# Kernel tuning notes

Measured on AMD Instinct MI355X. Metric: run time of the kernel, lower is better.

The kernel has to match this reference:

```python
import jax, jax.numpy as jnp
import numpy as np

TH = 0.01  # threshold from init
H = 56
W = 56


def setup_inputs() -> dict:
    key = jax.random.key(0)
    k1, k2 = jax.random.split(key)
    x = jax.random.uniform(k1, (32, 512, 56, 56), dtype=jnp.float32)
    conv_w = jax.random.normal(k2, (512, 1, 1, 1), dtype=jnp.float32)
    scale = jnp.ones((1,), dtype=jnp.float32)
    wf = jnp.ones((1,), dtype=jnp.float32)
    return {"x": x, "conv_w": conv_w, "scale": scale, "wf": wf}


def reference(x, conv_w, scale, wf):
    B, C, _, _ = x.shape
    # per-channel spatial mean: alpha[b,c] = sum_hw x / (H*W)
    alpha = jnp.sum(x, axis=(2, 3)) / (H * W)  # [B, C]
    # channel-weighted spatial sum, averaged over channels -> saliency [B, H, W]
    sal = jnp.einsum('bchw,bc->bhw', x, alpha) / C
    # conv1x1 with 1 input channel: broadcastmul by per-output-channel scalar
    w = conv_w.reshape(1, -1, 1, 1)                 # [1, Cout, 1, 1]
    fm = sal[:, None, :, :] * w                     # [B, Cout, H, W]
    fm = jax.nn.relu(fm)
    fm = jnp.where(fm > TH, fm, 0.0)                # nn.Threshold(th, 0)
    return 1.0 - wf * jax.nn.sigmoid(scale * fm)
```

## Files before the change

kernel.cpp:

```cpp
#include <hip/hip_runtime.h>
#include <hip/hip_bf16.h>

#define B 32
#define C 512
#define HW 3136
#define HW4 784
#define TH 0.01f
#define CPB 16
#define CPW 4
#define NPG 32

typedef float fx4 __attribute__((ext_vector_type(4)));

__global__ __launch_bounds__(256, 4) void partial_kernel(const float* __restrict__ x,
                                                         float* __restrict__ out) {
    const int b  = blockIdx.y;
    const int cg = blockIdx.x;
    const int t  = threadIdx.x;
    const int l  = t & 63;
    const int w  = t >> 6;

    const fx4* __restrict__ xb = (const fx4*)(x + (size_t)b * C * HW);

    fx4 acc[13];
    #pragma unroll
    for (int j = 0; j < 13; ++j) acc[j] = (fx4)0.f;

    const int cbase = cg * CPB + w * CPW;
    for (int i = 0; i < CPW; ++i) {
        const fx4* __restrict__ p = xb + (size_t)(cbase + i) * HW4;
        fx4 v[13];
        #pragma unroll
        for (int j = 0; j < 12; ++j) v[j] = __builtin_nontemporal_load(p + l + 64 * j);
        if (l < 16) v[12] = __builtin_nontemporal_load(p + l + 768);

        float s = 0.f;
        #pragma unroll
        for (int j = 0; j < 12; ++j) s += (v[j].x + v[j].y) + (v[j].z + v[j].w);
        if (l < 16) s += (v[12].x + v[12].y) + (v[12].z + v[12].w);
        #pragma unroll
        for (int off = 1; off < 64; off <<= 1) s += __shfl_xor(s, off);
        const float a = s * (1.0f / (float)HW);

        #pragma unroll
        for (int j = 0; j < 12; ++j) acc[j] += v[j] * a;
        if (l < 16) acc[12] += v[12] * a;
    }

    __shared__ fx4 lds[3][HW4];
    if (w > 0) {
        #pragma unroll
        for (int j = 0; j < 12; ++j) lds[w - 1][l + 64 * j] = acc[j];
        if (l < 16) lds[w - 1][l + 768] = acc[12];
    }
    __syncthreads();
    if (w == 0) {
        fx4* __restrict__ dst = (fx4*)(out + (size_t)b * C * HW) + (size_t)cg * HW4;
        #pragma unroll
        for (int j = 0; j < 12; ++j) {
            const int col = l + 64 * j;
            dst[col] = ((acc[j] + lds[0][col]) + (lds[1][col] + lds[2][col]));
        }
        if (l < 16) {
            const int col = l + 768;
            dst[col] = ((acc[12] + lds[0][col]) + (lds[1][col] + lds[2][col]));
        }
    }
}

__global__ __launch_bounds__(256) void out_kernel(const float* __restrict__ w,
                                                  const float* __restrict__ scale_p,
                                                  const float* __restrict__ wf_p,
                                                  float* __restrict__ out) {
    const int b    = blockIdx.y;
    const int tile = blockIdx.x;
    const int t    = threadIdx.x;
    const int hw4  = t & 15;
    const int pg2  = t >> 4;
    const int lane = t & 63;
    const int wid  = t >> 6;

    const fx4* __restrict__ P =
        (const fx4*)(out + (size_t)b * C * HW) + tile * 16 + hw4;
    fx4 s = P[(size_t)(2 * pg2) * HW4] + P[(size_t)(2 * pg2 + 1) * HW4];

    s.x += __shfl_xor(s.x, 16); s.y += __shfl_xor(s.y, 16);
    s.z += __shfl_xor(s.z, 16); s.w += __shfl_xor(s.w, 16);
    s.x += __shfl_xor(s.x, 32); s.y += __shfl_xor(s.y, 32);
    s.z += __shfl_xor(s.z, 32); s.w += __shfl_xor(s.w, 32);

    __shared__ fx4 red[4][16];
    if (lane < 16) red[wid][lane] = s;
    __syncthreads();

    __shared__ fx4 sal_sm[16];
    if (t < 16) {
        sal_sm[t] = ((red[0][t] + red[1][t]) + (red[2][t] + red[3][t])) *
                    (1.0f / (float)C);
    }
    __syncthreads();

    const float scale = scale_p[0];
    const float wf    = wf_p[0];
    const float out_zero = 1.0f - 0.5f * wf;
    const fx4 s4 = sal_sm[hw4];

    fx4* __restrict__ ob = (fx4*)(out + (size_t)b * C * HW) + tile * 16 + hw4;
    const int c0 = pg2 * 32;

    #pragma unroll 4
    for (int k = 0; k < 32; ++k) {
        const int co = c0 + k;
        const float wc = w[co];
        fx4 r;
        float fm;
        fm = s4.x * wc;
        r.x = (fm > TH) ? 1.0f - wf / (1.0f + __expf(-scale * fm)) : out_zero;
        fm = s4.y * wc;
        r.y = (fm > TH) ? 1.0f - wf / (1.0f + __expf(-scale * fm)) : out_zero;
        fm = s4.z * wc;
        r.z = (fm > TH) ? 1.0f - wf / (1.0f + __expf(-scale * fm)) : out_zero;
        fm = s4.w * wc;
        r.w = (fm > TH) ? 1.0f - wf / (1.0f + __expf(-scale * fm)) : out_zero;
        __builtin_nontemporal_store(r, ob + (size_t)co * HW4);
    }
}

extern "C" void kernel_launch(void* const* d_in, const int* in_sizes, int n_in,
                              void* d_out, int out_size, void* d_ws, size_t ws_size,
                              hipStream_t stream) {
    const float* x      = (const float*)d_in[0];
    const float* conv_w = (const float*)d_in[1];
    const float* scale  = (const float*)d_in[2];
    const float* wf     = (const float*)d_in[3];
    float* out = (float*)d_out;

    dim3 gridA(NPG, B);
    partial_kernel<<<gridA, 256, 0, stream>>>(x, out);

    dim3 gridB(HW4 / 16, B);
    out_kernel<<<gridB, 256, 0, stream>>>(conv_w, scale, wf, out);
}
```

Measured before the change: 88.29 us.

## Split saliency reduction into its own kernel and make output writes contiguous

Adds a separate kernel that sums the 32 partial saliency maps into a workspace buffer. The output kernel then stages the saliency row and the weights in LDS and writes a fully contiguous 8192-vector span per block, instead of 16-column strided tiles across channels. It also rewrites the per-channel sum in partial_kernel as a tree instead of a serial chain. The goal is more coalesced output stores and less latency from dependent adds, at the cost of an extra kernel launch and a workspace round trip.

```diff
diff --git a/kernel.cpp b/kernel.cpp
--- a/kernel.cpp
+++ b/kernel.cpp
@@ -34,10 +34,16 @@
         for (int j = 0; j < 12; ++j) v[j] = __builtin_nontemporal_load(p + l + 64 * j);
         if (l < 16) v[12] = __builtin_nontemporal_load(p + l + 768);
 
-        float s = 0.f;
+        float ps[12];
         #pragma unroll
-        for (int j = 0; j < 12; ++j) s += (v[j].x + v[j].y) + (v[j].z + v[j].w);
-        if (l < 16) s += (v[12].x + v[12].y) + (v[12].z + v[12].w);
+        for (int j = 0; j < 12; ++j) ps[j] = (v[j].x + v[j].y) + (v[j].z + v[j].w);
+        float s12 = 0.f;
+        if (l < 16) s12 = (v[12].x + v[12].y) + (v[12].z + v[12].w);
+        const float q0 = (ps[0] + ps[1]) + (ps[2] + ps[3]);
+        const float q1 = (ps[4] + ps[5]) + (ps[6] + ps[7]);
+        const float q2 = (ps[8] + ps[9]) + (ps[10] + ps[11]);
+        float s = (q0 + q1) + (q2 + s12);
+
         #pragma unroll
         for (int off = 1; off < 64; off <<= 1) s += __shfl_xor(s, off);
         const float a = s * (1.0f / (float)HW);
@@ -68,50 +74,52 @@
     }
 }
 
-__global__ __launch_bounds__(256) void out_kernel(const float* __restrict__ w,
+__global__ __launch_bounds__(256) void sal_reduce_kernel(const float* __restrict__ out,
+                                                         fx4* __restrict__ sal) {
+    const int b   = blockIdx.y;
+    const int col = blockIdx.x * 256 + threadIdx.x;
+    if (col >= HW4) return;
+    const fx4* __restrict__ P = (const fx4*)(out + (size_t)b * C * HW) + col;
+    fx4 s = (fx4)0.f;
+    #pragma unroll
+    for (int pg = 0; pg < NPG; ++pg) s += P[(size_t)pg * HW4];
+    sal[b * HW4 + col] = s * (1.0f / (float)C);
+}
+
+__global__ __launch_bounds__(256) void out_kernel(const fx4* __restrict__ sal,
+                                                  const float* __restrict__ w,
                                                   const float* __restrict__ scale_p,
                                                   const float* __restrict__ wf_p,
                                                   float* __restrict__ out) {
-    const int b    = blockIdx.y;
-    const int tile = blockIdx.x;
-    const int t    = threadIdx.x;
-    const int hw4  = t & 15;
-    const int pg2  = t >> 4;
-    const int lane = t & 63;
-    const int wid  = t >> 6;
+    const int b  = blockIdx.y;
+    const int t  = threadIdx.x;
+    const int F0 = blockIdx.x * 8192;
 
-    const fx4* __restrict__ P =
-        (const fx4*)(out + (size_t)b * C * HW) + tile * 16 + hw4;
-    fx4 s = P[(size_t)(2 * pg2) * HW4] + P[(size_t)(2 * pg2 + 1) * HW4];
-
-    s.x += __shfl_xor(s.x, 16); s.y += __shfl_xor(s.y, 16);
-    s.z += __shfl_xor(s.z, 16); s.w += __shfl_xor(s.w, 16);
-    s.x += __shfl_xor(s.x, 32); s.y += __shfl_xor(s.y, 32);
-    s.z += __shfl_xor(s.z, 32); s.w += __shfl_xor(s.w, 32);
-
-    __shared__ fx4 red[4][16];
-    if (lane < 16) red[wid][lane] = s;
-    __syncthreads();
-
-    __shared__ fx4 sal_sm[16];
-    if (t < 16) {
-        sal_sm[t] = ((red[0][t] + red[1][t]) + (red[2][t] + red[3][t])) *
-                    (1.0f / (float)C);
-    }
+    __shared__ fx4  sal_sm[HW4];
+    __shared__ float w_sm[C];
+    const fx4* __restrict__ sb = sal + b * HW4;
+    for (int i = t; i < HW4; i += 256) sal_sm[i] = sb[i];
+    for (int i = t; i < C;   i += 256) w_sm[i]  = w[i];
     __syncthreads();
 
     const float scale = scale_p[0];
     const float wf    = wf_p[0];
     const float out_zero = 1.0f - 0.5f * wf;
-    const fx4 s4 = sal_sm[hw4];
 
-    fx4* __restrict__ ob = (fx4*)(out + (size_t)b * C * HW) + tile * 16 + hw4;
-    const int c0 = pg2 * 32;
+    fx4* __restrict__ ob = (fx4*)(out + (size_t)b * C * HW) + F0;
 
-    #pragma unroll 4
-    for (int k = 0; k < 32; ++k) {
-        const int co = c0 + k;
-        const float wc = w[co];
+    int colb = F0 % HW4;
+    int cob  = F0 / HW4;
+
+    for (int it = 0; it < 32; ++it) {
+        int c = colb + t;
+        const int wrapped = (c >= HW4) ? 1 : 0;
+        c -= wrapped ? HW4 : 0;
+        const int co = cob + wrapped;
+
+        const fx4  s4 = sal_sm[c];
+        const float wc = w_sm[co];
+
         fx4 r;
         float fm;
         fm = s4.x * wc;
@@ -122,7 +130,10 @@
         r.z = (fm > TH) ? 1.0f - wf / (1.0f + __expf(-scale * fm)) : out_zero;
         fm = s4.w * wc;
         r.w = (fm > TH) ? 1.0f - wf / (1.0f + __expf(-scale * fm)) : out_zero;
-        __builtin_nontemporal_store(r, ob + (size_t)co * HW4);
+        __builtin_nontemporal_store(r, ob + it * 256 + t);
+
+        colb += 256;
+        if (colb >= HW4) { colb -= HW4; cob += 1; }
     }
 }
 
@@ -134,10 +145,14 @@
     const float* scale  = (const float*)d_in[2];
     const float* wf     = (const float*)d_in[3];
     float* out = (float*)d_out;
+    fx4*   sal = (fx4*)d_ws;
 
     dim3 gridA(NPG, B);
     partial_kernel<<<gridA, 256, 0, stream>>>(x, out);
 
-    dim3 gridB(HW4 / 16, B);
-    out_kernel<<<gridB, 256, 0, stream>>>(conv_w, scale, wf, out);
+    dim3 gridA2((HW4 + 255) / 256, B);
+    sal_reduce_kernel<<<gridA2, 256, 0, stream>>>(out, sal);
+
+    dim3 gridB(49, B);
+    out_kernel<<<gridB, 256, 0, stream>>>(sal, conv_w, scale, wf, out);
 }
```

New measurement: 96.32 us. +9.1%, slower.

## Split each channel's spatial plane across all four waves with block-level alpha reduction

Applied to the files above, without the earlier changes.

The partial kernel now has the four waves share each channel's spatial plane, each wave covering a quarter, instead of giving each wave whole channels. Per-channel sums are combined through a small double-buffered shared array with a block barrier per pair of channels. This removes the large LDS cross-wave reduction and cuts register use to four accumulators, at the cost of one __syncthreads per channel pair. Nontemporal loads are also dropped in favour of plain loads.

```diff
diff --git a/kernel.cpp b/kernel.cpp
--- a/kernel.cpp
+++ b/kernel.cpp
@@ -6,66 +6,67 @@
 #define HW 3136
 #define HW4 784
 #define TH 0.01f
+#define NPG 32
 #define CPB 16
-#define CPW 4
-#define NPG 32
 
 typedef float fx4 __attribute__((ext_vector_type(4)));
 
 __global__ __launch_bounds__(256, 4) void partial_kernel(const float* __restrict__ x,
                                                          float* __restrict__ out) {
     const int b  = blockIdx.y;
-    const int cg = blockIdx.x;
+    const int pg = blockIdx.x;
     const int t  = threadIdx.x;
     const int l  = t & 63;
-    const int w  = t >> 6;
+    const int wv = t >> 6;
 
-    const fx4* __restrict__ xb = (const fx4*)(x + (size_t)b * C * HW);
+    __shared__ float sums[2][2][4];
 
-    fx4 acc[13];
-    #pragma unroll
-    for (int j = 0; j < 13; ++j) acc[j] = (fx4)0.f;
+    const float* __restrict__ xb = x + (size_t)b * C * HW;
+    const int qbase = wv * 196;
 
-    const int cbase = cg * CPB + w * CPW;
-    for (int i = 0; i < CPW; ++i) {
-        const fx4* __restrict__ p = xb + (size_t)(cbase + i) * HW4;
-        fx4 v[13];
+    fx4 acc0 = (fx4)0.f, acc1 = (fx4)0.f, acc2 = (fx4)0.f, acc3 = (fx4)0.f;
+
+    #pragma unroll 2
+    for (int g = 0; g < 8; ++g) {
+        const int c0 = pg * CPB + 2 * g;
+        const fx4* __restrict__ p0 = (const fx4*)(xb + (size_t)c0 * HW) + qbase + l;
+        const fx4* __restrict__ p1 = (const fx4*)(xb + (size_t)(c0 + 1) * HW) + qbase + l;
+
+        const fx4 a0 = p0[0], a1 = p0[64], a2 = p0[128];
+        const fx4 b0 = p1[0], b1 = p1[64], b2 = p1[128];
+        fx4 a3 = (fx4)0.f, b3 = (fx4)0.f;
+        if (l < 4) { a3 = p0[192]; b3 = p1[192]; }
+
+        float sa = (((a0.x + a0.y) + (a0.z + a0.w)) + ((a1.x + a1.y) + (a1.z + a1.w))) +
+                   (((a2.x + a2.y) + (a2.z + a2.w)) + ((a3.x + a3.y) + (a3.z + a3.w)));
+        float sb = (((b0.x + b0.y) + (b0.z + b0.w)) + ((b1.x + b1.y) + (b1.z + b1.w))) +
+                   (((b2.x + b2.y) + (b2.z + b2.w)) + ((b3.x + b3.y) + (b3.z + b3.w)));
         #pragma unroll
-        for (int j = 0; j < 12; ++j) v[j] = __builtin_nontemporal_load(p + l + 64 * j);
-        if (l < 16) v[12] = __builtin_nontemporal_load(p + l + 768);
+        for (int off = 1; off < 64; off <<= 1) {
+            sa += __shfl_xor(sa, off);
+            sb += __shfl_xor(sb, off);
+        }
+        if (l == 0) {
+            sums[g & 1][0][wv] = sa;
+            sums[g & 1][1][wv] = sb;
+        }
+        __syncthreads();
+        const float al0 = ((sums[g & 1][0][0] + sums[g & 1][0][1]) +
+                           (sums[g & 1][0][2] + sums[g & 1][0][3])) * (1.0f / (float)HW);
+        const float al1 = ((sums[g & 1][1][0] + sums[g & 1][1][1]) +
+                           (sums[g & 1][1][2] + sums[g & 1][1][3])) * (1.0f / (float)HW);
 
-        float s = 0.f;
-        #pragma unroll
-        for (int j = 0; j < 12; ++j) s += (v[j].x + v[j].y) + (v[j].z + v[j].w);
-        if (l < 16) s += (v[12].x + v[12].y) + (v[12].z + v[12].w);
-        #pragma unroll
-        for (int off = 1; off < 64; off <<= 1) s += __shfl_xor(s, off);
-        const float a = s * (1.0f / (float)HW);
-
-        #pragma unroll
-        for (int j = 0; j < 12; ++j) acc[j] += v[j] * a;
-        if (l < 16) acc[12] += v[12] * a;
+        acc0 += a0 * al0 + b0 * al1;
+        acc1 += a1 * al0 + b1 * al1;
+        acc2 += a2 * al0 + b2 * al1;
+        acc3 += a3 * al0 + b3 * al1;
     }
 
-    __shared__ fx4 lds[3][HW4];
-    if (w > 0) {
-        #pragma unroll
-        for (int j = 0; j < 12; ++j) lds[w - 1][l + 64 * j] = acc[j];
-        if (l < 16) lds[w - 1][l + 768] = acc[12];
-    }
-    __syncthreads();
-    if (w == 0) {
-        fx4* __restrict__ dst = (fx4*)(out + (size_t)b * C * HW) + (size_t)cg * HW4;
-        #pragma unroll
-        for (int j = 0; j < 12; ++j) {
-            const int col = l + 64 * j;
-            dst[col] = ((acc[j] + lds[0][col]) + (lds[1][col] + lds[2][col]));
-        }
-        if (l < 16) {
-            const int col = l + 768;
-            dst[col] = ((acc[12] + lds[0][col]) + (lds[1][col] + lds[2][col]));
-        }
-    }
+    fx4* __restrict__ dst = (fx4*)(out + (size_t)b * C * HW + (size_t)pg * HW) + qbase + l;
+    dst[0]   = acc0;
+    dst[64]  = acc1;
+    dst[128] = acc2;
+    if (l < 4) dst[192] = acc3;
 }
 
 __global__ __launch_bounds__(256) void out_kernel(const float* __restrict__ w,
```

New measurement: 82.90 us. -6.1%, faster.
